# Performance work log

Measured on AMD Instinct MI355X. Metric: run time of the kernel, lower is better.

Reference implementation:

```python
import jax, jax.numpy as jnp
import numpy as np

B, LQ, LK, DIM = 2, 2048, 2048, 1024
HEADS, DH = 8, 64
INNER = HEADS * DH  # 512


def setup_inputs() -> dict:
    key = jax.random.key(0)
    ks = jax.random.split(key, 7)
    x = jax.random.normal(ks[0], (B, LQ, DIM), dtype=jnp.float32)
    y = jax.random.normal(ks[1], (B, LK, DIM), dtype=jnp.float32)
    # binary mask, 1 => masked (gets -1e9 added)
    mask = jax.random.randint(ks[2], (B, LQ, LK), 0, 2).astype(jnp.float32)
    s = 0.02
    Wq = jax.random.normal(ks[3], (INNER, DIM), dtype=jnp.float32) * s
    Wk = jax.random.normal(ks[4], (INNER, DIM), dtype=jnp.float32) * s
    Wv = jax.random.normal(ks[5], (INNER, DIM), dtype=jnp.float32) * s
    Wo = jax.random.normal(ks[6], (DIM, INNER), dtype=jnp.float32) * s
    return {"x": x, "y": y, "mask": mask, "Wq": Wq, "Wk": Wk, "Wv": Wv, "Wo": Wo}


def reference(x, y, mask, Wq, Wk, Wv, Wo):
    scale = DH ** -0.5
    # projections (Linear without bias: x @ W.T)
    q = (x @ Wq.T) * scale            # [B, LQ, INNER]
    k = y @ Wk.T                      # [B, LK, INNER]
    v = y @ Wv.T                      # [B, LK, INNER]
    # split into heads (torch.split along last dim == reshape to [.., H, DH])
    q = q.reshape(B, LQ, HEADS, DH)
    k = k.reshape(B, LK, HEADS, DH)
    v = v.reshape(B, LK, HEADS, DH)
    # per-head QK^T + additive mask*-1e9, softmax over keys, then V
    scores = jnp.einsum('bqhd,bkhd->bhqk', q, k) + mask[:, None, :, :] * (-1e9)
    attn = jax.nn.softmax(scores, axis=-1)
    out = jnp.einsum('bhqk,bkhd->bqhd', attn, v).reshape(B, LQ, INNER)
    return out @ Wo.T                 # [B, LQ, DIM]
```

## Files before the change

kernel.cpp:

```cpp
#include <hip/hip_runtime.h>
#include <hip/hip_bf16.h>
#include <stdint.h>

#define BATCH 2
#define LQ 2048
#define LK 2048
#define DIM 1024
#define HEADS 8
#define DH 64
#define INNER 512

typedef __attribute__((ext_vector_type(8))) short short8;
typedef __attribute__((ext_vector_type(4))) float f32x4;

__device__ __forceinline__ float bf2f(unsigned short u) {
    union { unsigned int i; float f; } v;
    v.i = ((unsigned int)u) << 16;
    return v.f;
}
__device__ __forceinline__ unsigned short f2bf(float f) {
    __hip_bfloat16 h = __float2bfloat16(f);
    return *reinterpret_cast<unsigned short*>(&h);
}
__device__ __forceinline__ float fexp2(float x) {
#if __has_builtin(__builtin_amdgcn_exp2f)
    return __builtin_amdgcn_exp2f(x);
#else
    return __expf(x * 0.69314718056f);
#endif
}
__device__ __forceinline__ void stc(unsigned short* C, size_t i, float v) { C[i] = f2bf(v); }
__device__ __forceinline__ void stc(float* C, size_t i, float v) { C[i] = v; }

typedef __attribute__((address_space(1))) const unsigned int gu32;
typedef __attribute__((address_space(3))) unsigned int lu32;
__device__ __forceinline__ void gload16(const void* g, void* l) {
    __builtin_amdgcn_global_load_lds((gu32*)g, (lu32*)l, 16, 0, 0);
}

__global__ __launch_bounds__(256) void prep(
    const float* __restrict__ x,  const float* __restrict__ y,
    const float* __restrict__ wq, const float* __restrict__ wk,
    const float* __restrict__ wv, const float* __restrict__ wo,
    const float* __restrict__ mask,
    unsigned short* __restrict__ xb,  unsigned short* __restrict__ yb,
    unsigned short* __restrict__ wqb, unsigned short* __restrict__ wkb,
    unsigned short* __restrict__ wvb, unsigned short* __restrict__ wob,
    unsigned long long* __restrict__ mbits)
{
    if (blockIdx.y == 6) {
        const int wid = blockIdx.x * 4 + (threadIdx.x >> 6);
        const int lane = threadIdx.x & 63;
        for (int task = wid; task < BATCH * LQ * 8; task += 4096) {
            int row = task >> 3, g = task & 7;
            const float* mp = mask + (size_t)row * LK + g * 256;
            unsigned long long* ob = mbits + (size_t)row * (LK / 64) + g * 4;
            float v0 = mp[0 * 64 + lane];
            float v1 = mp[1 * 64 + lane];
            float v2 = mp[2 * 64 + lane];
            float v3 = mp[3 * 64 + lane];
            unsigned long long b0 = __ballot(v0 > 0.5f);
            unsigned long long b1 = __ballot(v1 > 0.5f);
            unsigned long long b2 = __ballot(v2 > 0.5f);
            unsigned long long b3 = __ballot(v3 > 0.5f);
            if (lane == 0) { ob[0] = b0; ob[1] = b1; ob[2] = b2; ob[3] = b3; }
        }
        return;
    }
    const float* src; unsigned short* dst; int n4;
    switch (blockIdx.y) {
        case 0: src = x;  dst = xb;  n4 = (BATCH * LQ * DIM) / 4; break;
        case 1: src = y;  dst = yb;  n4 = (BATCH * LK * DIM) / 4; break;
        case 2: src = wq; dst = wqb; n4 = (INNER * DIM) / 4; break;
        case 3: src = wk; dst = wkb; n4 = (INNER * DIM) / 4; break;
        case 4: src = wv; dst = wvb; n4 = (INNER * DIM) / 4; break;
        default: src = wo; dst = wob; n4 = (INNER * DIM) / 4; break;
    }
    const int stride = gridDim.x * 256;
    for (int i = blockIdx.x * 256 + threadIdx.x; i < n4; i += stride) {
        float4 f = ((const float4*)src)[i];
        ushort4 u;
        u.x = f2bf(f.x); u.y = f2bf(f.y); u.z = f2bf(f.z); u.w = f2bf(f.w);
        ((ushort4*)dst)[i] = u;
    }
}

template <int IM, int JN, typename TC, int EPI>
__device__ __forceinline__ void gemm_body(
    const unsigned short* __restrict__ A,
    const unsigned short* __restrict__ W,
    TC* __restrict__ C,
    int K, int N, float scale,
    unsigned short* As, unsigned short* Bs)
{
    constexpr int BM = IM * 32;
    constexpr int BN = JN * 32;
    constexpr int ACH = BM * 8;
    constexpr int BCH = BN * 8;
    constexpr int AUS = BM * 64;
    constexpr int BUS = BN * 64;

    const int tid = threadIdx.x;
    const int m0 = blockIdx.x * BM;
    const int n0 = blockIdx.y * BN;
    const int w = tid >> 6, lane = tid & 63;
    const int q4 = lane >> 4, l16 = lane & 15;
    const int wm = (w >> 1) * (IM * 16), wn = (w & 1) * (JN * 16);
    const int sw = l16 & 7;

    f32x4 acc[IM][JN] = {};

#pragma unroll
    for (int i = 0; i < ACH / 256; ++i) {
        int s = tid + i * 256;
        int r = s >> 3, ch = (s & 7) ^ (r & 7);
        gload16(A + (size_t)(m0 + r) * K + ch * 8, As + (size_t)s * 8);
    }
#pragma unroll
    for (int i = 0; i < BCH / 256; ++i) {
        int s = tid + i * 256;
        int r = s >> 3, ch = (s & 7) ^ (r & 7);
        gload16(W + (size_t)(n0 + r) * K + ch * 8, Bs + (size_t)s * 8);
    }
    __syncthreads();

    const int nt = K / 64;
    for (int t = 0; t < nt; ++t) {
        const int curA = (t & 1) * AUS;
        const int curB = (t & 1) * BUS;
        if (t + 1 < nt) {
            int kk = (t + 1) * 64;
            const int nxtA = AUS - curA, nxtB = BUS - curB;
#pragma unroll
            for (int i = 0; i < ACH / 256; ++i) {
                int s = tid + i * 256;
                int r = s >> 3, ch = (s & 7) ^ (r & 7);
                gload16(A + (size_t)(m0 + r) * K + kk + ch * 8, As + nxtA + (size_t)s * 8);
            }
#pragma unroll
            for (int i = 0; i < BCH / 256; ++i) {
                int s = tid + i * 256;
                int r = s >> 3, ch = (s & 7) ^ (r & 7);
                gload16(W + (size_t)(n0 + r) * K + kk + ch * 8, Bs + nxtB + (size_t)s * 8);
            }
        }

#pragma unroll
        for (int ks = 0; ks < 2; ++ks) {
            const int kq = ((ks * 4 + q4) ^ sw) * 8;
            short8 a[IM], b[JN];
#pragma unroll
            for (int i = 0; i < IM; ++i)
                a[i] = *(const short8*)(As + curA + (wm + i * 16 + l16) * 64 + kq);
#pragma unroll
            for (int j = 0; j < JN; ++j)
                b[j] = *(const short8*)(Bs + curB + (wn + j * 16 + l16) * 64 + kq);
#pragma unroll
            for (int i = 0; i < IM; ++i)
#pragma unroll
                for (int j = 0; j < JN; ++j)
                    acc[i][j] = __builtin_amdgcn_mfma_f32_16x16x32_bf16(
                        a[i], b[j], acc[i][j], 0, 0, 0);
        }
        __syncthreads();
    }

    if (EPI == 0) {
#pragma unroll
        for (int i = 0; i < IM; ++i)
#pragma unroll
            for (int j = 0; j < JN; ++j)
#pragma unroll
                for (int r = 0; r < 4; ++r) {
                    int row = m0 + wm + i * 16 + q4 * 4 + r;
                    int col = n0 + wn + j * 16 + l16;
                    stc(C, (size_t)row * N + col, acc[i][j][r] * scale);
                }
    } else {
        constexpr int KW = IM * 16;
        constexpr int DW = JN * 16;
        constexpr int TPS = KW + 8;
        unsigned short* TP = As + w * (DW * TPS);
#pragma unroll
        for (int i = 0; i < IM; ++i)
#pragma unroll
            for (int j = 0; j < JN; ++j) {
                ushort4 u;
                u.x = f2bf(acc[i][j][0]); u.y = f2bf(acc[i][j][1]);
                u.z = f2bf(acc[i][j][2]); u.w = f2bf(acc[i][j][3]);
                *(ushort4*)(TP + (j * 16 + l16) * TPS + i * 16 + q4 * 4) = u;
            }
        const int keyflat = m0 + wm;
        const int bb = keyflat >> 11, key0 = keyflat & (LK - 1);
        const int hh = (n0 + wn) >> 6;
        const int dlow = (n0 + wn) & 63;
        constexpr int RCH = KW / 8;
        constexpr int NCH = DW * RCH;
#pragma unroll
        for (int p = 0; p < NCH / 64; ++p) {
            int c = p * 64 + lane;
            int dl = c / RCH, kc = c % RCH;
            uint4 v = *(const uint4*)(TP + dl * TPS + kc * 8);
            *(uint4*)((unsigned short*)C +
                ((size_t)((bb * HEADS + hh) * DH + dlow + dl)) * LK + key0 + kc * 8) = v;
        }
    }
}

#define QSCALE 0.18033688011112042f

__global__ __launch_bounds__(256) void proj_qkv(
    const unsigned short* __restrict__ xb, const unsigned short* __restrict__ yb,
    const unsigned short* __restrict__ wqb, const unsigned short* __restrict__ wkb,
    const unsigned short* __restrict__ wvb,
    unsigned short* __restrict__ qb, unsigned short* __restrict__ kb,
    unsigned short* __restrict__ vt)
{
    __shared__ __align__(16) unsigned short As[2 * 128 * 64];
    __shared__ __align__(16) unsigned short Bs[2 * 64 * 64];
    const int z = blockIdx.z;
    const unsigned short* A = (z == 0) ? xb : yb;
    const unsigned short* W = (z == 0) ? wqb : (z == 1) ? wkb : wvb;
    if (z == 2)
        gemm_body<4, 2, unsigned short, 1>(A, W, vt, DIM, INNER, 1.0f, As, Bs);
    else
        gemm_body<4, 2, unsigned short, 0>(A, W, (z == 0) ? qb : kb, DIM, INNER,
                                           (z == 0) ? QSCALE : 1.0f, As, Bs);
}

__global__ __launch_bounds__(256) void gemm_out(
    const unsigned short* __restrict__ A,
    const unsigned short* __restrict__ W,
    float* __restrict__ C)
{
    __shared__ __align__(16) unsigned short As[2 * 128 * 64];
    __shared__ __align__(16) unsigned short Bs[2 * 64 * 64];
    gemm_body<4, 2, float, 0>(A, W, C, INNER, DIM, 1.0f, As, Bs);
}

#define AT_US (64 * 64)

__global__ __launch_bounds__(256) void attn_mfma(
    const unsigned short* __restrict__ Q,
    const unsigned short* __restrict__ Kb,
    const unsigned short* __restrict__ Vt,
    const unsigned long long* __restrict__ Mb,
    unsigned short* __restrict__ O)
{
    __shared__ __align__(16) unsigned short Ks[2 * AT_US];
    __shared__ __align__(16) unsigned short Vs[2 * AT_US];
    __shared__ __align__(16) unsigned short Ps[4][16 * 72];

    const int tid = threadIdx.x;
    const int q0 = blockIdx.x * 64;
    const int h = blockIdx.y, b = blockIdx.z;
    const int w = tid >> 6, lane = tid & 63;
    const int q4 = lane >> 4, l16 = lane & 15;
    const int sw = l16 & 7;

    short8 qf[2];
    {
        const unsigned short* qp =
            Q + (size_t)(b * LQ + q0 + w * 16 + l16) * INNER + h * DH + q4 * 8;
        qf[0] = *(const short8*)(qp);
        qf[1] = *(const short8*)(qp + 32);
    }

    f32x4 o[4] = {};
    float lacc[4] = {0.f, 0.f, 0.f, 0.f};

    const unsigned short* kbase = Kb + (size_t)(b * LK) * INNER + h * DH;
    const unsigned short* vbase = Vt + (size_t)((b * HEADS + h) * DH) * LK;
    const unsigned long long* mrow =
        Mb + (size_t)(b * LQ + q0 + w * 16 + q4 * 4) * (LK / 64);

    const int r0 = tid >> 3, ch0 = (tid & 7) ^ (r0 & 7);
    const int s1 = tid + 256;
    const int r1 = s1 >> 3, ch1 = (s1 & 7) ^ (r1 & 7);

    gload16(kbase + (size_t)r0 * INNER + ch0 * 8, Ks + (size_t)tid * 8);
    gload16(kbase + (size_t)r1 * INNER + ch1 * 8, Ks + (size_t)s1 * 8);
    gload16(vbase + (size_t)r0 * LK + ch0 * 8, Vs + (size_t)tid * 8);
    gload16(vbase + (size_t)r1 * LK + ch1 * 8, Vs + (size_t)s1 * 8);
    __syncthreads();

    const int NT = LK / 64;
    for (int t = 0; t < NT; ++t) {
        const int cur = (t & 1) * AT_US;
        if (t + 1 < NT) {
            const int nxt = AT_US - cur;
            int kn = (t + 1) * 64;
            gload16(kbase + (size_t)(kn + r0) * INNER + ch0 * 8, Ks + nxt + (size_t)tid * 8);
            gload16(kbase + (size_t)(kn + r1) * INNER + ch1 * 8, Ks + nxt + (size_t)s1 * 8);
            gload16(vbase + (size_t)r0 * LK + kn + ch0 * 8, Vs + nxt + (size_t)tid * 8);
            gload16(vbase + (size_t)r1 * LK + kn + ch1 * 8, Vs + nxt + (size_t)s1 * 8);
        }

        f32x4 s[4];
#pragma unroll
        for (int j = 0; j < 4; ++j) {
            s[j] = f32x4{0.f, 0.f, 0.f, 0.f};
#pragma unroll
            for (int ks = 0; ks < 2; ++ks) {
                short8 kf = *(const short8*)(Ks + cur + (j * 16 + l16) * 64
                                             + (((ks * 4 + q4) ^ sw) * 8));
                s[j] = __builtin_amdgcn_mfma_f32_16x16x32_bf16(qf[ks], kf, s[j], 0, 0, 0);
            }
        }

#pragma unroll
        for (int r = 0; r < 4; ++r) {
            unsigned long long bits = mrow[(size_t)r * (LK / 64) + t];
#pragma unroll
            for (int j = 0; j < 4; ++j) {
                float e = fexp2(s[j][r]);
                float pe = ((bits >> (j * 16 + l16)) & 1ull) ? 0.f : e;
                s[j][r] = pe;
                lacc[r] += pe;
            }
        }

#pragma unroll
        for (int j = 0; j < 4; ++j)
#pragma unroll
            for (int r = 0; r < 4; ++r)
                Ps[w][(q4 * 4 + r) * 72 + j * 16 + l16] = f2bf(s[j][r]);

#pragma unroll
        for (int ks = 0; ks < 2; ++ks) {
            short8 pf = *(const short8*)(&Ps[w][l16 * 72 + ks * 32 + q4 * 8]);
#pragma unroll
            for (int dd = 0; dd < 4; ++dd) {
                short8 vf = *(const short8*)(Vs + cur + (dd * 16 + l16) * 64
                                             + (((ks * 4 + q4) ^ sw) * 8));
                o[dd] = __builtin_amdgcn_mfma_f32_16x16x32_bf16(pf, vf, o[dd], 0, 0, 0);
            }
        }
        __syncthreads();
    }

#pragma unroll
    for (int off = 1; off < 16; off <<= 1)
#pragma unroll
        for (int r = 0; r < 4; ++r)
            lacc[r] += __shfl_xor(lacc[r], off);
    float inv[4];
#pragma unroll
    for (int r = 0; r < 4; ++r) inv[r] = 1.0f / lacc[r];

#pragma unroll
    for (int dd = 0; dd < 4; ++dd)
#pragma unroll
        for (int r = 0; r < 4; ++r) {
            int qrow = b * LQ + q0 + w * 16 + q4 * 4 + r;
            int col = h * DH + dd * 16 + l16;
            O[(size_t)qrow * INNER + col] = f2bf(o[dd][r] * inv[r]);
        }
}

extern "C" void kernel_launch(void* const* d_in, const int* in_sizes, int n_in,
                              void* d_out, int out_size, void* d_ws, size_t ws_size,
                              hipStream_t stream) {
    const float* x    = (const float*)d_in[0];
    const float* y    = (const float*)d_in[1];
    const float* mask = (const float*)d_in[2];
    const float* Wq   = (const float*)d_in[3];
    const float* Wk   = (const float*)d_in[4];
    const float* Wv   = (const float*)d_in[5];
    const float* Wo   = (const float*)d_in[6];
    float* out = (float*)d_out;

    const size_t NX = (size_t)BATCH * LQ * DIM;
    const size_t NS = (size_t)BATCH * LQ * INNER;
    const size_t NW = (size_t)INNER * DIM;
    unsigned short* xb  = (unsigned short*)d_ws;
    unsigned short* yb  = xb + NX;
    unsigned short* qb  = yb + NX;
    unsigned short* kb  = qb + NS;
    unsigned short* vt  = kb + NS;
    unsigned short* wqb = vt + NS;
    unsigned short* wkb = wqb + NW;
    unsigned short* wvb = wkb + NW;
    unsigned short* wob = wvb + NW;
    unsigned long long* mbits = (unsigned long long*)(wob + NW);
    unsigned short* ao  = xb;

    dim3 blk(256);
    prep<<<dim3(1024, 7), blk, 0, stream>>>(
        x, y, Wq, Wk, Wv, Wo, mask, xb, yb, wqb, wkb, wvb, wob, mbits);
    proj_qkv<<<dim3(4096 / 128, INNER / 64, 3), blk, 0, stream>>>(
        xb, yb, wqb, wkb, wvb, qb, kb, vt);
    attn_mfma<<<dim3(LQ / 64, HEADS, BATCH), blk, 0, stream>>>(
        qb, kb, vt, mbits, ao);
    gemm_out<<<dim3(4096 / 128, DIM / 64), blk, 0, stream>>>(ao, wob, out);
}
```

Before: 192.9 us.

## Split attention key loop across two wave groups with 512-thread blocks

The attention kernel now runs 512 threads per block. Two groups of four waves each process alternating 64-key tiles from a four-slot K/V ring buffer, then merge partial outputs and row sums through shared memory. This halves the serial key-loop length per block and raises waves per CU, which should hide latency better. The P scratch buffer also switches from padded rows to an XOR-swizzled layout to avoid bank conflicts. The cost is more LDS per block and a final reduction pass.

```diff
diff --git a/kernel.cpp b/kernel.cpp
--- a/kernel.cpp
+++ b/kernel.cpp
@@ -238,30 +238,32 @@
     gemm_body<4, 2, float, 0>(A, W, C, INNER, DIM, 1.0f, As, Bs);
 }
 
-#define AT_US (64 * 64)
-
-__global__ __launch_bounds__(256) void attn_mfma(
+#define AT_SLOT (64 * 64)
+
+__global__ __launch_bounds__(512, 4) void attn_mfma(
     const unsigned short* __restrict__ Q,
     const unsigned short* __restrict__ Kb,
     const unsigned short* __restrict__ Vt,
     const unsigned long long* __restrict__ Mb,
     unsigned short* __restrict__ O)
 {
-    __shared__ __align__(16) unsigned short Ks[2 * AT_US];
-    __shared__ __align__(16) unsigned short Vs[2 * AT_US];
-    __shared__ __align__(16) unsigned short Ps[4][16 * 72];
+    __shared__ __align__(16) unsigned short Ks[4 * AT_SLOT];
+    __shared__ __align__(16) unsigned short Vs[4 * AT_SLOT];
+    __shared__ __align__(16) unsigned short Ps[8 * 16 * 64];
 
     const int tid = threadIdx.x;
     const int q0 = blockIdx.x * 64;
     const int h = blockIdx.y, b = blockIdx.z;
     const int w = tid >> 6, lane = tid & 63;
+    const int g = w & 3;
+    const int par = w >> 2;
     const int q4 = lane >> 4, l16 = lane & 15;
     const int sw = l16 & 7;
 
     short8 qf[2];
     {
         const unsigned short* qp =
-            Q + (size_t)(b * LQ + q0 + w * 16 + l16) * INNER + h * DH + q4 * 8;
+            Q + (size_t)(b * LQ + q0 + g * 16 + l16) * INNER + h * DH + q4 * 8;
         qf[0] = *(const short8*)(qp);
         qf[1] = *(const short8*)(qp + 32);
     }
@@ -272,29 +274,35 @@
     const unsigned short* kbase = Kb + (size_t)(b * LK) * INNER + h * DH;
     const unsigned short* vbase = Vt + (size_t)((b * HEADS + h) * DH) * LK;
     const unsigned long long* mrow =
-        Mb + (size_t)(b * LQ + q0 + w * 16 + q4 * 4) * (LK / 64);
-
-    const int r0 = tid >> 3, ch0 = (tid & 7) ^ (r0 & 7);
-    const int s1 = tid + 256;
-    const int r1 = s1 >> 3, ch1 = (s1 & 7) ^ (r1 & 7);
-
-    gload16(kbase + (size_t)r0 * INNER + ch0 * 8, Ks + (size_t)tid * 8);
-    gload16(kbase + (size_t)r1 * INNER + ch1 * 8, Ks + (size_t)s1 * 8);
-    gload16(vbase + (size_t)r0 * LK + ch0 * 8, Vs + (size_t)tid * 8);
-    gload16(vbase + (size_t)r1 * LK + ch1 * 8, Vs + (size_t)s1 * 8);
+        Mb + (size_t)(b * LQ + q0 + g * 16 + q4 * 4) * (LK / 64);
+
+    const int rr = tid >> 3;
+    const int ch = (tid & 7) ^ (rr & 7);
+
+#pragma unroll
+    for (int tn = 0; tn < 2; ++tn) {
+        gload16(kbase + (size_t)(tn * 64 + rr) * INNER + ch * 8,
+                Ks + tn * AT_SLOT + (size_t)tid * 8);
+        gload16(vbase + (size_t)rr * LK + tn * 64 + ch * 8,
+                Vs + tn * AT_SLOT + (size_t)tid * 8);
+    }
     __syncthreads();
 
-    const int NT = LK / 64;
-    for (int t = 0; t < NT; ++t) {
-        const int cur = (t & 1) * AT_US;
-        if (t + 1 < NT) {
-            const int nxt = AT_US - cur;
-            int kn = (t + 1) * 64;
-            gload16(kbase + (size_t)(kn + r0) * INNER + ch0 * 8, Ks + nxt + (size_t)tid * 8);
-            gload16(kbase + (size_t)(kn + r1) * INNER + ch1 * 8, Ks + nxt + (size_t)s1 * 8);
-            gload16(vbase + (size_t)r0 * LK + kn + ch0 * 8, Vs + nxt + (size_t)tid * 8);
-            gload16(vbase + (size_t)r1 * LK + kn + ch1 * 8, Vs + nxt + (size_t)s1 * 8);
-        }
+    const int NR = LK / 128;
+    for (int rd = 0; rd < NR; ++rd) {
+        if (rd + 1 < NR) {
+#pragma unroll
+            for (int i = 0; i < 2; ++i) {
+                const int tn = 2 * rd + 2 + i;
+                const int sl = tn & 3;
+                gload16(kbase + (size_t)(tn * 64 + rr) * INNER + ch * 8,
+                        Ks + sl * AT_SLOT + (size_t)tid * 8);
+                gload16(vbase + (size_t)rr * LK + tn * 64 + ch * 8,
+                        Vs + sl * AT_SLOT + (size_t)tid * 8);
+            }
+        }
+        const int t = 2 * rd + par;
+        const int cur = (t & 3) * AT_SLOT;
 
         f32x4 s[4];
 #pragma unroll
@@ -309,26 +317,30 @@
         }
 
 #pragma unroll
-        for (int r = 0; r < 4; ++r) {
-            unsigned long long bits = mrow[(size_t)r * (LK / 64) + t];
+        for (int r2 = 0; r2 < 4; ++r2) {
+            unsigned long long bits = mrow[(size_t)r2 * (LK / 64) + t];
 #pragma unroll
             for (int j = 0; j < 4; ++j) {
-                float e = fexp2(s[j][r]);
+                float e = fexp2(s[j][r2]);
                 float pe = ((bits >> (j * 16 + l16)) & 1ull) ? 0.f : e;
-                s[j][r] = pe;
-                lacc[r] += pe;
-            }
-        }
-
+                s[j][r2] = pe;
+                lacc[r2] += pe;
+            }
+        }
+
+        unsigned short* Pw = Ps + w * 1024;
 #pragma unroll
         for (int j = 0; j < 4; ++j)
 #pragma unroll
-            for (int r = 0; r < 4; ++r)
-                Ps[w][(q4 * 4 + r) * 72 + j * 16 + l16] = f2bf(s[j][r]);
+            for (int r2 = 0; r2 < 4; ++r2) {
+                const int row = q4 * 4 + r2;
+                Pw[row * 64 + (((j * 2 + (l16 >> 3)) ^ (row & 7)) << 3) + (l16 & 7)]
+                    = f2bf(s[j][r2]);
+            }
 
 #pragma unroll
         for (int ks = 0; ks < 2; ++ks) {
-            short8 pf = *(const short8*)(&Ps[w][l16 * 72 + ks * 32 + q4 * 8]);
+            short8 pf = *(const short8*)(Pw + l16 * 64 + (((ks * 4 + q4) ^ sw) << 3));
 #pragma unroll
             for (int dd = 0; dd < 4; ++dd) {
                 short8 vf = *(const short8*)(Vs + cur + (dd * 16 + l16) * 64
@@ -339,23 +351,44 @@
         __syncthreads();
     }
 
-#pragma unroll
-    for (int off = 1; off < 16; off <<= 1)
-#pragma unroll
-        for (int r = 0; r < 4; ++r)
-            lacc[r] += __shfl_xor(lacc[r], off);
-    float inv[4];
-#pragma unroll
-    for (int r = 0; r < 4; ++r) inv[r] = 1.0f / lacc[r];
-
-#pragma unroll
-    for (int dd = 0; dd < 4; ++dd)
-#pragma unroll
-        for (int r = 0; r < 4; ++r) {
-            int qrow = b * LQ + q0 + w * 16 + q4 * 4 + r;
-            int col = h * DH + dd * 16 + l16;
-            O[(size_t)qrow * INNER + col] = f2bf(o[dd][r] * inv[r]);
-        }
+    float* xch = (float*)Ks;
+    if (par) {
+        float* d = xch + (size_t)(g * 64 + lane) * 21;
+#pragma unroll
+        for (int dd = 0; dd < 4; ++dd)
+#pragma unroll
+            for (int r2 = 0; r2 < 4; ++r2) d[dd * 4 + r2] = o[dd][r2];
+#pragma unroll
+        for (int r2 = 0; r2 < 4; ++r2) d[16 + r2] = lacc[r2];
+    }
+    __syncthreads();
+    if (!par) {
+        const float* d = xch + (size_t)(g * 64 + lane) * 21;
+#pragma unroll
+        for (int dd = 0; dd < 4; ++dd)
+#pragma unroll
+            for (int r2 = 0; r2 < 4; ++r2) o[dd][r2] += d[dd * 4 + r2];
+#pragma unroll
+        for (int r2 = 0; r2 < 4; ++r2) lacc[r2] += d[16 + r2];
+
+#pragma unroll
+        for (int off = 1; off < 16; off <<= 1)
+#pragma unroll
+            for (int r2 = 0; r2 < 4; ++r2)
+                lacc[r2] += __shfl_xor(lacc[r2], off);
+        float inv[4];
+#pragma unroll
+        for (int r2 = 0; r2 < 4; ++r2) inv[r2] = 1.0f / lacc[r2];
+
+#pragma unroll
+        for (int dd = 0; dd < 4; ++dd)
+#pragma unroll
+            for (int r2 = 0; r2 < 4; ++r2) {
+                int qrow = b * LQ + q0 + g * 16 + q4 * 4 + r2;
+                int col = h * DH + dd * 16 + l16;
+                O[(size_t)qrow * INNER + col] = f2bf(o[dd][r2] * inv[r2]);
+            }
+    }
 }
 
 extern "C" void kernel_launch(void* const* d_in, const int* in_sizes, int n_in,
@@ -390,7 +423,7 @@
         x, y, Wq, Wk, Wv, Wo, mask, xb, yb, wqb, wkb, wvb, wob, mbits);
     proj_qkv<<<dim3(4096 / 128, INNER / 64, 3), blk, 0, stream>>>(
         xb, yb, wqb, wkb, wvb, qb, kb, vt);
-    attn_mfma<<<dim3(LQ / 64, HEADS, BATCH), blk, 0, stream>>>(
+    attn_mfma<<<dim3(LQ / 64, HEADS, BATCH), dim3(512), 0, stream>>>(
         qb, kb, vt, mbits, ao);
     gemm_out<<<dim3(4096 / 128, DIM / 64), blk, 0, stream>>>(ao, wob, out);
 }
```

Measured after the change: 183.7 us. 4.8% less time.
